# Kernel tuning notes

Hardware: AMD Instinct MI355X
Metric: run time of the kernel (lower is better)

The kernel has to match this reference:

```python
import jax, jax.numpy as jnp
import numpy as np

NUM_LEVELS = 16
LEVEL_DIM = 2
BASE_RES = 32
PER_LEVEL_SCALE = 2.0
TABLE_SIZE = 2 ** 19  # padded size of every level's table
RES = np.array([int(BASE_RES * PER_LEVEL_SCALE ** i) for i in range(NUM_LEVELS)], dtype=np.float32)
SIZES = np.minimum(RES.astype(np.float64) ** 3, TABLE_SIZE).astype(np.float32)  # true table sizes
NEAR, FAR, NUM_SAMPLES = 0.1, 1.5, 64
N_RAYS = 16384


def _xavier(key, fin, fout):
    lim = float(np.sqrt(6.0 / (fin + fout)))
    return jax.random.uniform(key, (fin, fout), jnp.float32, -lim, lim)


def setup_inputs() -> dict:
    key = jax.random.key(0)
    ks = jax.random.split(key, 12)
    rays_o = jax.random.uniform(ks[0], (N_RAYS, 3), jnp.float32, -0.5, 0.5)
    d = jax.random.normal(ks[1], (N_RAYS, 3), jnp.float32)
    rays_d = d / jnp.linalg.norm(d, axis=-1, keepdims=True)
    tables = jax.random.uniform(ks[2], (NUM_LEVELS, TABLE_SIZE, LEVEL_DIM), jnp.float32, -1e-4, 1e-4)
    return {
        'rays_o': rays_o, 'rays_d': rays_d, 'tables': tables,
        'Wg0': _xavier(ks[3], 32, 64), 'bg0': jnp.zeros((64,), jnp.float32),
        'Wg1': _xavier(ks[4], 64, 64), 'bg1': jnp.zeros((64,), jnp.float32),
        'Wd': _xavier(ks[5], 64, 16), 'bd': jnp.zeros((16,), jnp.float32),
        'Wc0': _xavier(ks[6], 24, 64), 'bc0': jnp.zeros((64,), jnp.float32),
        'Wc1': _xavier(ks[7], 64, 64), 'bc1': jnp.zeros((64,), jnp.float32),
        'Wc2': _xavier(ks[8], 64, 64), 'bc2': jnp.zeros((64,), jnp.float32),
        'Wch': _xavier(ks[9], 64, 3), 'bch': jnp.zeros((3,), jnp.float32),
    }


def _hash_encode(pts, tables):
    # pts: [N, S, 3] in roughly [-1, 1]; tables: [L, T, 2]
    res = jnp.asarray(RES)            # [L]
    sizes = jnp.asarray(SIZES)        # [L]
    scaled = (pts[..., None, :] + 1.0) / 2.0 * (res[:, None] - 1.0)     # [N,S,L,3]
    scaled = jnp.clip(scaled, 0.0, res[:, None] - 1.0)
    # torch computes the flat index in float then .long() (truncation), then clamps to table size
    idx_f = scaled[..., 0] * res * res + scaled[..., 1] * res + scaled[..., 2]  # [N,S,L]
    idx = jnp.minimum(idx_f, sizes - 1.0).astype(jnp.int32)
    feats = tables[jnp.arange(NUM_LEVELS)[None, None, :], idx]          # [N,S,L,2]
    return feats.reshape(feats.shape[:-2] + (NUM_LEVELS * LEVEL_DIM,))  # [N,S,32]


def _sh_encode(d):
    # degree-4 encoder in the source only ever builds 9 features
    x, y, z = d[..., 0], d[..., 1], d[..., 2]
    return jnp.stack([jnp.full_like(x, 0.5), x, y, z,
                      x * y, x * z, y * z, x * x - y * y, 3.0 * z * z - 1.0], axis=-1)  # [N,9]


def reference(rays_o, rays_d, tables, Wg0, bg0, Wg1, bg1, Wd, bd,
              Wc0, bc0, Wc1, bc1, Wc2, bc2, Wch, bch):
    n = rays_o.shape[0]
    # --- stratified-free (eval mode) sampling along rays ---
    t = jnp.linspace(0.0, 1.0, NUM_SAMPLES, dtype=jnp.float32)
    z_vals = jnp.broadcast_to(NEAR + (FAR - NEAR) * t, (n, NUM_SAMPLES))           # [N,S]
    pts = rays_o[:, None, :] + rays_d[:, None, :] * z_vals[..., None]              # [N,S,3]
    # --- LoDAwareNeRF forward ---
    feats = _hash_encode(pts, tables)                                              # [N,S,32]
    h = jax.nn.relu(feats @ Wg0 + bg0)
    h = jax.nn.relu(h @ Wg1 + bg1)
    geo = h @ Wd + bd                                                              # [N,S,16]
    density = jax.nn.softplus(geo[..., 0] - 1.0)                                   # [N,S]
    geo_feat = geo[..., 1:]                                                        # [N,S,15]
    dir_f = jnp.broadcast_to(_sh_encode(rays_d)[:, None, :], (n, NUM_SAMPLES, 9))  # [N,S,9]
    c = jnp.concatenate([geo_feat, dir_f], axis=-1)                                # [N,S,24]
    c = jax.nn.relu(c @ Wc0 + bc0)
    c = jax.nn.relu(c @ Wc1 + bc1)
    c = jax.nn.relu(c @ Wc2 + bc2)
    color = jax.nn.sigmoid(c @ Wch + bch)                                          # [N,S,3]
    # --- volume rendering compositing ---
    dists = z_vals[..., 1:] - z_vals[..., :-1]
    dists = jnp.concatenate([dists, jnp.full_like(dists[..., :1], 1e10)], axis=-1)
    dists = dists * jnp.linalg.norm(rays_d, axis=-1, keepdims=True)
    alpha = 1.0 - jnp.exp(-density * dists)                                        # [N,S]
    T = jnp.cumprod(1.0 - alpha + 1e-10, axis=-1)
    T = jnp.concatenate([jnp.ones_like(T[..., :1]), T[..., :-1]], axis=-1)
    weights = alpha * T                                                            # [N,S]
    rgb = jnp.sum(weights[..., None] * color, axis=-2)                             # [N,3]
    depth = jnp.sum(weights * z_vals, axis=-1)                                     # [N]
    acc = jnp.sum(weights, axis=-1)                                                # [N]
    return rgb, depth, acc, weights
```

## Files before the change

kernel.cpp:

```cpp
#include <hip/hip_runtime.h>
#include <hip/hip_bf16.h>
#include <math.h>

typedef float  f32x4 __attribute__((ext_vector_type(4)));
typedef short  s16x8 __attribute__((ext_vector_type(8)));
typedef unsigned int u32x2 __attribute__((ext_vector_type(2)));
typedef unsigned int u32x4 __attribute__((ext_vector_type(4)));

constexpr int kNRays = 16384;
constexpr int kTableSize = 1 << 19;
constexpr int kOffDepth   = kNRays * 3;
constexpr int kOffAcc     = kOffDepth + kNRays;
constexpr int kOffWeights = kOffAcc + kNRays;

constexpr int kWg0 = 0;
constexpr int kWg1 = 2048;
constexpr int kWd  = 6144;
constexpr int kWc0 = 7168;
constexpr int kWc1 = 9216;
constexpr int kWc2 = 13312;
constexpr int kWch = 17408;
constexpr int kWsTotal = 18432;

__device__ __forceinline__ ushort f2bf(float x) {
    unsigned u = __float_as_uint(x);
    return (ushort)((u + 0x7FFFu + ((u >> 16) & 1u)) >> 16);
}
__device__ __forceinline__ unsigned pk2(float lo, float hi) {
    __hip_bfloat162 h = __float22bfloat162_rn(float2{lo, hi});
    return *reinterpret_cast<unsigned*>(&h);
}
__device__ __forceinline__ float sel4(float v0, float v1, float v2, float v3, int s) {
    float a = (s & 1) ? v1 : v0;
    float b = (s & 1) ? v3 : v2;
    return (s & 2) ? b : a;
}
__device__ __forceinline__ float wave_sum(float v) {
#pragma unroll
    for (int off = 32; off > 0; off >>= 1) v += __shfl_xor(v, off, 64);
    return v;
}

__global__ __launch_bounds__(256) void prep_weights(
    const float* __restrict__ Wg0, const float* __restrict__ Wg1,
    const float* __restrict__ Wd,  const float* __restrict__ Wc0,
    const float* __restrict__ Wc1, const float* __restrict__ Wc2,
    const float* __restrict__ Wch, ushort* __restrict__ ws)
{
    const int i = blockIdx.x * 256 + threadIdx.x;
    if (i >= kWsTotal) return;
    const float* W; int FIN, FOUT, KT, base; bool dperm = false;
    if (i < kWg1)      { W = Wg0; FIN = 32; FOUT = 64; KT = 1; base = kWg0; }
    else if (i < kWd)  { W = Wg1; FIN = 64; FOUT = 64; KT = 2; base = kWg1; }
    else if (i < kWc0) { W = Wd;  FIN = 64; FOUT = 16; KT = 2; base = kWd; dperm = true; }
    else if (i < kWc1) { W = Wc0; FIN = 24; FOUT = 64; KT = 1; base = kWc0; }
    else if (i < kWc2) { W = Wc1; FIN = 64; FOUT = 64; KT = 2; base = kWc1; }
    else if (i < kWch) { W = Wc2; FIN = 64; FOUT = 64; KT = 2; base = kWc2; }
    else               { W = Wch; FIN = 64; FOUT = 3;  KT = 2; base = kWch; }
    const int r = i - base;
    const int e = r & 7, l = (r >> 3) & 63, t = r >> 9;
    const int kt = t % KT, mt = t / KT;
    const int k = kt * 32 + ((l >> 4) << 3) + e;
    int j = mt * 16 + (l & 15);
    if (dperm) j = (j == 15) ? 0 : j + 1;
    float w = 0.0f;
    if (k < FIN && j < FOUT) w = W[k * FOUT + j];
    ws[i] = f2bf(w);
}

template<int KT, bool RELU>
__device__ __forceinline__ void layer64(ushort* Xw, const ushort* __restrict__ Aws,
                                        const float* __restrict__ bias,
                                        int c16, int g, int lane) {
    s16x8 B[KT][4];
#pragma unroll
    for (int kt = 0; kt < KT; ++kt)
#pragma unroll
        for (int nt = 0; nt < 4; ++nt) {
            const int col = nt * 16 + c16;
            B[kt][nt] = *(const s16x8*)&Xw[col * 64 + 8 * ((kt * 4 + g) ^ (c16 & 7))];
        }
#pragma unroll
    for (int mt = 0; mt < 4; ++mt) {
        const s16x8 A0 = *(const s16x8*)&Aws[((mt * KT + 0) * 64 + lane) * 8];
        s16x8 A1;
        if constexpr (KT == 2) A1 = *(const s16x8*)&Aws[((mt * KT + 1) * 64 + lane) * 8];
        const f32x4 b = *(const f32x4*)(bias + mt * 16 + g * 4);
        f32x4 acc[4];
#pragma unroll
        for (int nt = 0; nt < 4; ++nt) {
            acc[nt] = b;
            acc[nt] = __builtin_amdgcn_mfma_f32_16x16x32_bf16(A0, B[0][nt], acc[nt], 0, 0, 0);
            if constexpr (KT == 2)
                acc[nt] = __builtin_amdgcn_mfma_f32_16x16x32_bf16(A1, B[1][nt], acc[nt], 0, 0, 0);
        }
#pragma unroll
        for (int nt = 0; nt < 4; ++nt) {
            const int col = nt * 16 + c16;
            float x0 = acc[nt].x, x1 = acc[nt].y, x2 = acc[nt].z, x3 = acc[nt].w;
            if (RELU) {
                x0 = fmaxf(x0, 0.f); x1 = fmaxf(x1, 0.f);
                x2 = fmaxf(x2, 0.f); x3 = fmaxf(x3, 0.f);
            }
            const int a = col * 64 + 8 * ((2 * mt + (g >> 1)) ^ (c16 & 7)) + 4 * (g & 1);
            *(u32x2*)&Xw[a] = (u32x2){ pk2(x0, x1), pk2(x2, x3) };
        }
    }
}

template<int KT>
__device__ __forceinline__ void layer16(const ushort* Xw, const ushort* __restrict__ Aws,
                                        int c16, int g, int lane, f32x4 acc[4]) {
    const s16x8 A0 = *(const s16x8*)&Aws[(0 * 64 + lane) * 8];
    s16x8 A1;
    if constexpr (KT == 2) A1 = *(const s16x8*)&Aws[(1 * 64 + lane) * 8];
#pragma unroll
    for (int nt = 0; nt < 4; ++nt) {
        const int col = nt * 16 + c16;
        const s16x8 B0 = *(const s16x8*)&Xw[col * 64 + 8 * ((0 * 4 + g) ^ (c16 & 7))];
        acc[nt] = __builtin_amdgcn_mfma_f32_16x16x32_bf16(A0, B0, acc[nt], 0, 0, 0);
        if constexpr (KT == 2) {
            const s16x8 B1 = *(const s16x8*)&Xw[col * 64 + 8 * ((1 * 4 + g) ^ (c16 & 7))];
            acc[nt] = __builtin_amdgcn_mfma_f32_16x16x32_bf16(A1, B1, acc[nt], 0, 0, 0);
        }
    }
}

__global__ __launch_bounds__(256, 4) void nerf_mfma_kernel(
    const float* __restrict__ rays_o, const float* __restrict__ rays_d,
    const float* __restrict__ tables, const ushort* __restrict__ ws,
    const float* __restrict__ bg0, const float* __restrict__ bg1,
    const float* __restrict__ bd,  const float* __restrict__ bc0,
    const float* __restrict__ bc1, const float* __restrict__ bc2,
    const float* __restrict__ bch, float* __restrict__ out)
{
    __shared__ __align__(16) ushort Xs[4 * 4096];
    const int tid  = threadIdx.x;
    const int wid  = tid >> 6;
    const int lane = tid & 63;
    const int c16  = lane & 15;
    const int g    = lane >> 4;
    const int ray  = blockIdx.x * 4 + wid;
    ushort* Xw = Xs + wid * 4096;

    const float ox = rays_o[ray * 3 + 0], oy = rays_o[ray * 3 + 1], oz = rays_o[ray * 3 + 2];
    const float dx = rays_d[ray * 3 + 0], dy = rays_d[ray * 3 + 1], dz = rays_d[ray * 3 + 2];

    const float step = 1.0f / 63.0f;
    const float z  = 0.1f + 1.4f * ((float)lane * step);
    const float zn = 0.1f + 1.4f * ((float)(lane + 1) * step);

    s16x8 B0[4];
#pragma unroll
    for (int nt = 0; nt < 4; ++nt) {
        const int s = nt * 16 + c16;
        const float zs = 0.1f + 1.4f * ((float)s * step);
        const float px = ox + dx * zs, py = oy + dy * zs, pz = oz + dz * zs;
        u32x4 val;
#pragma unroll
        for (int j = 0; j < 4; ++j) {
            const int lv = g * 4 + j;
            const float res = (float)(32 << lv);
            const float rm1 = res - 1.0f;
            float sx = (px + 1.0f) * 0.5f * rm1; sx = fminf(fmaxf(sx, 0.f), rm1);
            float sy = (py + 1.0f) * 0.5f * rm1; sy = fminf(fmaxf(sy, 0.f), rm1);
            float sz = (pz + 1.0f) * 0.5f * rm1; sz = fminf(fmaxf(sz, 0.f), rm1);
            const float idxf = sx * res * res + sy * res + sz;
            const float szm1 = (lv == 0) ? 32767.f : (lv == 1) ? 262143.f : 524287.f;
            const int idx = (int)fminf(idxf, szm1);
            const float2 f2 = *reinterpret_cast<const float2*>(
                tables + ((size_t)lv * kTableSize + (size_t)idx) * 2);
            val[j] = pk2(f2.x, f2.y);
        }
        B0[nt] = *(const s16x8*)&val;
    }

#pragma unroll
    for (int mt = 0; mt < 4; ++mt) {
        const s16x8 A0 = *(const s16x8*)&ws[kWg0 + (mt * 64 + lane) * 8];
        const f32x4 b = *(const f32x4*)(bg0 + mt * 16 + g * 4);
        f32x4 acc[4];
#pragma unroll
        for (int nt = 0; nt < 4; ++nt) {
            acc[nt] = b;
            acc[nt] = __builtin_amdgcn_mfma_f32_16x16x32_bf16(A0, B0[nt], acc[nt], 0, 0, 0);
        }
#pragma unroll
        for (int nt = 0; nt < 4; ++nt) {
            const int col = nt * 16 + c16;
            const float x0 = fmaxf(acc[nt].x, 0.f), x1 = fmaxf(acc[nt].y, 0.f);
            const float x2 = fmaxf(acc[nt].z, 0.f), x3 = fmaxf(acc[nt].w, 0.f);
            const int a = col * 64 + 8 * ((2 * mt + (g >> 1)) ^ (c16 & 7)) + 4 * (g & 1);
            *(u32x2*)&Xw[a] = (u32x2){ pk2(x0, x1), pk2(x2, x3) };
        }
    }

    layer64<2, true>(Xw, ws + kWg1, bg1, c16, g, lane);

    f32x4 accd[4];
    {
        const float db0 = bd[g * 4 + 1];
        const float db1 = bd[g * 4 + 2];
        const float db2 = bd[g * 4 + 3];
        const int i3 = (g == 3) ? 0 : g * 4 + 4;
        const float db3 = bd[i3];
        const f32x4 b = { db0, db1, db2, db3 };
#pragma unroll
        for (int nt = 0; nt < 4; ++nt) accd[nt] = b;
    }
    layer16<2>(Xw, ws + kWd, c16, g, lane, accd);
    const float lgit = sel4(__shfl(accd[0].w, 48 + c16, 64),
                            __shfl(accd[1].w, 48 + c16, 64),
                            __shfl(accd[2].w, 48 + c16, 64),
                            __shfl(accd[3].w, 48 + c16, 64), g);
#pragma unroll
    for (int nt = 0; nt < 4; ++nt) {
        const int col = nt * 16 + c16;
        const int a = col * 64 + 8 * ((g >> 1) ^ (c16 & 7)) + 4 * (g & 1);
        *(u32x2*)&Xw[a] = (u32x2){ pk2(accd[nt].x, accd[nt].y), pk2(accd[nt].z, accd[nt].w) };
    }
    Xw[lane * 64 + 8 * (1 ^ (lane & 7)) + 7] = 0x3F00;
    {
        u32x4 w = { pk2(dx, dy), pk2(dz, dx * dy), pk2(dx * dz, dy * dz),
                    pk2(dx * dx - dy * dy, 3.f * dz * dz - 1.f) };
        *(u32x4*)&Xw[lane * 64 + 8 * (2 ^ (lane & 7))] = w;
    }

    layer64<1, true>(Xw, ws + kWc0, bc0, c16, g, lane);
    layer64<2, true>(Xw, ws + kWc1, bc1, c16, g, lane);
    layer64<2, true>(Xw, ws + kWc2, bc2, c16, g, lane);

    f32x4 accc[4];
    {
        const float cb0 = bch[0], cb1 = bch[1], cb2 = bch[2];
        const f32x4 b = (g == 0) ? (f32x4){ cb0, cb1, cb2, 0.f } : (f32x4){ 0.f, 0.f, 0.f, 0.f };
#pragma unroll
        for (int nt = 0; nt < 4; ++nt) accc[nt] = b;
    }
    layer16<2>(Xw, ws + kWch, c16, g, lane, accc);
    const float lr = sel4(__shfl(accc[0].x, c16, 64), __shfl(accc[1].x, c16, 64),
                          __shfl(accc[2].x, c16, 64), __shfl(accc[3].x, c16, 64), g);
    const float lgr = sel4(__shfl(accc[0].y, c16, 64), __shfl(accc[1].y, c16, 64),
                           __shfl(accc[2].y, c16, 64), __shfl(accc[3].y, c16, 64), g);
    const float lb = sel4(__shfl(accc[0].z, c16, 64), __shfl(accc[1].z, c16, 64),
                          __shfl(accc[2].z, c16, 64), __shfl(accc[3].z, c16, 64), g);

    const float cr = 1.f / (1.f + expf(-lr));
    const float cg = 1.f / (1.f + expf(-lgr));
    const float cb = 1.f / (1.f + expf(-lb));
    const float gx = lgit - 1.0f;
    const float density = fmaxf(gx, 0.f) + log1pf(expf(-fabsf(gx)));

    const float dnorm = sqrtf(dx * dx + dy * dy + dz * dz);
    float dist = (lane < 63) ? (zn - z) : 1e10f;
    dist *= dnorm;
    const float alpha = 1.0f - expf(-density * dist);
    float f = 1.0f - alpha + 1e-10f;
#pragma unroll
    for (int off = 1; off < 64; off <<= 1) {
        const float gg = __shfl_up(f, off, 64);
        if (lane >= off) f *= gg;
    }
    float T = __shfl_up(f, 1, 64);
    if (lane == 0) T = 1.0f;
    const float w = alpha * T;

    out[kOffWeights + ray * 64 + lane] = w;
    const float sr = wave_sum(w * cr);
    const float sg = wave_sum(w * cg);
    const float sb = wave_sum(w * cb);
    const float sd = wave_sum(w * z);
    const float sa = wave_sum(w);
    if (lane == 0) {
        out[ray * 3 + 0] = sr;
        out[ray * 3 + 1] = sg;
        out[ray * 3 + 2] = sb;
        out[kOffDepth + ray] = sd;
        out[kOffAcc + ray]   = sa;
    }
}

extern "C" void kernel_launch(void* const* d_in, const int* in_sizes, int n_in,
                              void* d_out, int out_size, void* d_ws, size_t ws_size,
                              hipStream_t stream) {
    const float* rays_o = (const float*)d_in[0];
    const float* rays_d = (const float*)d_in[1];
    const float* tables = (const float*)d_in[2];
    const float* Wg0 = (const float*)d_in[3];
    const float* bg0 = (const float*)d_in[4];
    const float* Wg1 = (const float*)d_in[5];
    const float* bg1 = (const float*)d_in[6];
    const float* Wd  = (const float*)d_in[7];
    const float* bd  = (const float*)d_in[8];
    const float* Wc0 = (const float*)d_in[9];
    const float* bc0 = (const float*)d_in[10];
    const float* Wc1 = (const float*)d_in[11];
    const float* bc1 = (const float*)d_in[12];
    const float* Wc2 = (const float*)d_in[13];
    const float* bc2 = (const float*)d_in[14];
    const float* Wch = (const float*)d_in[15];
    const float* bch = (const float*)d_in[16];
    float* out = (float*)d_out;
    ushort* wsp = (ushort*)d_ws;

    prep_weights<<<dim3((kWsTotal + 255) / 256), dim3(256), 0, stream>>>(
        Wg0, Wg1, Wd, Wc0, Wc1, Wc2, Wch, wsp);

    nerf_mfma_kernel<<<dim3(kNRays / 4), dim3(256), 0, stream>>>(
        rays_o, rays_d, tables, wsp,
        bg0, bg1, bd, bc0, bc1, bc2, bch, out);
}
```

Measured before the change: 80.55 us.

## Shrink blocks to two waves, fold color bias into weights, add MFMA priority

Launches 128-thread blocks handling two rays each instead of 256-thread blocks with four rays, raising the occupancy hint to 6 blocks per SIMD-group. It folds the bc0 bias into the Wc0 weight matrix via a constant-one input column, so the bias load is removed. It wraps MFMA sequences in s_setprio so matrix work is prioritized. It also rewrites the hash-coordinate arithmetic with fma and fmed3 and precomputes per-level table base pointers. These cut scalar ALU and load overhead but add scheduling-priority effects and small bf16 rounding of the bias.

```diff
diff --git a/kernel.cpp b/kernel.cpp
--- a/kernel.cpp
+++ b/kernel.cpp
@@ -45,15 +45,16 @@
     const float* __restrict__ Wg0, const float* __restrict__ Wg1,
     const float* __restrict__ Wd,  const float* __restrict__ Wc0,
     const float* __restrict__ Wc1, const float* __restrict__ Wc2,
-    const float* __restrict__ Wch, ushort* __restrict__ ws)
+    const float* __restrict__ Wch, const float* __restrict__ bc0,
+    ushort* __restrict__ ws)
 {
     const int i = blockIdx.x * 256 + threadIdx.x;
     if (i >= kWsTotal) return;
-    const float* W; int FIN, FOUT, KT, base; bool dperm = false;
+    const float* W; int FIN, FOUT, KT, base; bool dperm = false, c0bias = false;
     if (i < kWg1)      { W = Wg0; FIN = 32; FOUT = 64; KT = 1; base = kWg0; }
     else if (i < kWd)  { W = Wg1; FIN = 64; FOUT = 64; KT = 2; base = kWg1; }
     else if (i < kWc0) { W = Wd;  FIN = 64; FOUT = 16; KT = 2; base = kWd; dperm = true; }
-    else if (i < kWc1) { W = Wc0; FIN = 24; FOUT = 64; KT = 1; base = kWc0; }
+    else if (i < kWc1) { W = Wc0; FIN = 24; FOUT = 64; KT = 1; base = kWc0; c0bias = true; }
     else if (i < kWc2) { W = Wc1; FIN = 64; FOUT = 64; KT = 2; base = kWc1; }
     else if (i < kWch) { W = Wc2; FIN = 64; FOUT = 64; KT = 2; base = kWc2; }
     else               { W = Wch; FIN = 64; FOUT = 3;  KT = 2; base = kWch; }
@@ -65,10 +66,11 @@
     if (dperm) j = (j == 15) ? 0 : j + 1;
     float w = 0.0f;
     if (k < FIN && j < FOUT) w = W[k * FOUT + j];
+    if (c0bias && k == 24 && j < FOUT) w = bc0[j];
     ws[i] = f2bf(w);
 }
 
-template<int KT, bool RELU>
+template<int KT, bool RELU, bool HASBIAS>
 __device__ __forceinline__ void layer64(ushort* Xw, const ushort* __restrict__ Aws,
                                         const float* __restrict__ bias,
                                         int c16, int g, int lane) {
@@ -85,8 +87,11 @@
         const s16x8 A0 = *(const s16x8*)&Aws[((mt * KT + 0) * 64 + lane) * 8];
         s16x8 A1;
         if constexpr (KT == 2) A1 = *(const s16x8*)&Aws[((mt * KT + 1) * 64 + lane) * 8];
-        const f32x4 b = *(const f32x4*)(bias + mt * 16 + g * 4);
+        f32x4 b;
+        if constexpr (HASBIAS) b = *(const f32x4*)(bias + mt * 16 + g * 4);
+        else                   b = (f32x4){ 0.f, 0.f, 0.f, 0.f };
         f32x4 acc[4];
+        __builtin_amdgcn_s_setprio(1);
 #pragma unroll
         for (int nt = 0; nt < 4; ++nt) {
             acc[nt] = b;
@@ -94,6 +99,7 @@
             if constexpr (KT == 2)
                 acc[nt] = __builtin_amdgcn_mfma_f32_16x16x32_bf16(A1, B[1][nt], acc[nt], 0, 0, 0);
         }
+        __builtin_amdgcn_s_setprio(0);
 #pragma unroll
         for (int nt = 0; nt < 4; ++nt) {
             const int col = nt * 16 + c16;
@@ -114,6 +120,7 @@
     const s16x8 A0 = *(const s16x8*)&Aws[(0 * 64 + lane) * 8];
     s16x8 A1;
     if constexpr (KT == 2) A1 = *(const s16x8*)&Aws[(1 * 64 + lane) * 8];
+    __builtin_amdgcn_s_setprio(1);
 #pragma unroll
     for (int nt = 0; nt < 4; ++nt) {
         const int col = nt * 16 + c16;
@@ -124,23 +131,24 @@
             acc[nt] = __builtin_amdgcn_mfma_f32_16x16x32_bf16(A1, B1, acc[nt], 0, 0, 0);
         }
     }
-}
-
-__global__ __launch_bounds__(256, 4) void nerf_mfma_kernel(
+    __builtin_amdgcn_s_setprio(0);
+}
+
+__global__ __launch_bounds__(128, 6) void nerf_mfma_kernel(
     const float* __restrict__ rays_o, const float* __restrict__ rays_d,
     const float* __restrict__ tables, const ushort* __restrict__ ws,
     const float* __restrict__ bg0, const float* __restrict__ bg1,
-    const float* __restrict__ bd,  const float* __restrict__ bc0,
-    const float* __restrict__ bc1, const float* __restrict__ bc2,
-    const float* __restrict__ bch, float* __restrict__ out)
+    const float* __restrict__ bd,  const float* __restrict__ bc1,
+    const float* __restrict__ bc2, const float* __restrict__ bch,
+    float* __restrict__ out)
 {
-    __shared__ __align__(16) ushort Xs[4 * 4096];
+    __shared__ __align__(16) ushort Xs[2 * 4096];
     const int tid  = threadIdx.x;
     const int wid  = tid >> 6;
     const int lane = tid & 63;
     const int c16  = lane & 15;
     const int g    = lane >> 4;
-    const int ray  = blockIdx.x * 4 + wid;
+    const int ray  = blockIdx.x * 2 + wid;
     ushort* Xw = Xs + wid * 4096;
 
     const float ox = rays_o[ray * 3 + 0], oy = rays_o[ray * 3 + 1], oz = rays_o[ray * 3 + 2];
@@ -150,26 +158,32 @@
     const float z  = 0.1f + 1.4f * ((float)lane * step);
     const float zn = 0.1f + 1.4f * ((float)(lane + 1) * step);
 
+    const float2* lvb[4];
+#pragma unroll
+    for (int j = 0; j < 4; ++j)
+        lvb[j] = (const float2*)tables + ((size_t)(g * 4 + j) << 19);
+
+    const float tc = (float)c16 * step;
     s16x8 B0[4];
 #pragma unroll
     for (int nt = 0; nt < 4; ++nt) {
-        const int s = nt * 16 + c16;
-        const float zs = 0.1f + 1.4f * ((float)s * step);
-        const float px = ox + dx * zs, py = oy + dy * zs, pz = oz + dz * zs;
+        const float ts = tc + (float)nt * (16.0f / 63.0f);
+        const float zs = fmaf(1.4f, ts, 0.1f);
+        const float px = fmaf(dx, zs, ox), py = fmaf(dy, zs, oy), pz = fmaf(dz, zs, oz);
         u32x4 val;
 #pragma unroll
         for (int j = 0; j < 4; ++j) {
             const int lv = g * 4 + j;
             const float res = (float)(32 << lv);
             const float rm1 = res - 1.0f;
-            float sx = (px + 1.0f) * 0.5f * rm1; sx = fminf(fmaxf(sx, 0.f), rm1);
-            float sy = (py + 1.0f) * 0.5f * rm1; sy = fminf(fmaxf(sy, 0.f), rm1);
-            float sz = (pz + 1.0f) * 0.5f * rm1; sz = fminf(fmaxf(sz, 0.f), rm1);
-            const float idxf = sx * res * res + sy * res + sz;
+            const float h = 0.5f * rm1;
+            const float sx = __builtin_amdgcn_fmed3f(fmaf(px, h, h), 0.f, rm1);
+            const float sy = __builtin_amdgcn_fmed3f(fmaf(py, h, h), 0.f, rm1);
+            const float sz = __builtin_amdgcn_fmed3f(fmaf(pz, h, h), 0.f, rm1);
+            const float idxf = fmaf(sx, res * res, fmaf(sy, res, sz));
             const float szm1 = (lv == 0) ? 32767.f : (lv == 1) ? 262143.f : 524287.f;
             const int idx = (int)fminf(idxf, szm1);
-            const float2 f2 = *reinterpret_cast<const float2*>(
-                tables + ((size_t)lv * kTableSize + (size_t)idx) * 2);
+            const float2 f2 = lvb[j][idx];
             val[j] = pk2(f2.x, f2.y);
         }
         B0[nt] = *(const s16x8*)&val;
@@ -180,11 +194,13 @@
         const s16x8 A0 = *(const s16x8*)&ws[kWg0 + (mt * 64 + lane) * 8];
         const f32x4 b = *(const f32x4*)(bg0 + mt * 16 + g * 4);
         f32x4 acc[4];
+        __builtin_amdgcn_s_setprio(1);
 #pragma unroll
         for (int nt = 0; nt < 4; ++nt) {
             acc[nt] = b;
             acc[nt] = __builtin_amdgcn_mfma_f32_16x16x32_bf16(A0, B0[nt], acc[nt], 0, 0, 0);
         }
+        __builtin_amdgcn_s_setprio(0);
 #pragma unroll
         for (int nt = 0; nt < 4; ++nt) {
             const int col = nt * 16 + c16;
@@ -195,7 +211,7 @@
         }
     }
 
-    layer64<2, true>(Xw, ws + kWg1, bg1, c16, g, lane);
+    layer64<2, true, true>(Xw, ws + kWg1, bg1, c16, g, lane);
 
     f32x4 accd[4];
     {
@@ -225,10 +241,14 @@
                     pk2(dx * dx - dy * dy, 3.f * dz * dz - 1.f) };
         *(u32x4*)&Xw[lane * 64 + 8 * (2 ^ (lane & 7))] = w;
     }
-
-    layer64<1, true>(Xw, ws + kWc0, bc0, c16, g, lane);
-    layer64<2, true>(Xw, ws + kWc1, bc1, c16, g, lane);
-    layer64<2, true>(Xw, ws + kWc2, bc2, c16, g, lane);
+    {
+        u32x4 w = { 0x00003F80u, 0u, 0u, 0u };
+        *(u32x4*)&Xw[lane * 64 + 8 * (3 ^ (lane & 7))] = w;
+    }
+
+    layer64<1, true, false>(Xw, ws + kWc0, nullptr, c16, g, lane);
+    layer64<2, true, true >(Xw, ws + kWc1, bc1, c16, g, lane);
+    layer64<2, true, true >(Xw, ws + kWc2, bc2, c16, g, lane);
 
     f32x4 accc[4];
     {
@@ -304,9 +324,9 @@
     ushort* wsp = (ushort*)d_ws;
 
     prep_weights<<<dim3((kWsTotal + 255) / 256), dim3(256), 0, stream>>>(
-        Wg0, Wg1, Wd, Wc0, Wc1, Wc2, Wch, wsp);
-
-    nerf_mfma_kernel<<<dim3(kNRays / 4), dim3(256), 0, stream>>>(
+        Wg0, Wg1, Wd, Wc0, Wc1, Wc2, Wch, bc0, wsp);
+
+    nerf_mfma_kernel<<<dim3(kNRays / 2), dim3(128), 0, stream>>>(
         rays_o, rays_d, tables, wsp,
-        bg0, bg1, bd, bc0, bc1, bc2, bch, out);
-}
+        bg0, bg1, bd, bc1, bc2, bch, out);
+}
```

New measurement: 84.18 us. 1.05x slower.
